# Kernel optimization log

Hardware: AMD Instinct MI355X
Metric: run time of the kernel (lower is better)

The kernel has to match this reference:

```python
import jax, jax.numpy as jnp
import numpy as np

B, T, C = 2, 2048, 1024
H, D, R = 16, 64, 32  # heads, head_dim, compression rank (R < D)


def setup_inputs() -> dict:
    key = jax.random.key(0)
    ks = jax.random.split(key, 8)
    s = 0.02
    return {
        "hidden_states": jax.random.normal(ks[0], (B, T, C), jnp.float32),
        "c_attn_w": jax.random.normal(ks[1], (C, 3 * C), jnp.float32) * s,
        "c_attn_b": jnp.zeros((3 * C,), jnp.float32),
        "c_proj_w": jax.random.normal(ks[2], (C, C), jnp.float32) * s,
        "c_proj_b": jnp.zeros((C,), jnp.float32),
        "wk_c": jax.random.normal(ks[3], (D, R), jnp.float32) * (1.0 / np.sqrt(D)),
        "wk_e": jax.random.normal(ks[4], (R, D), jnp.float32) * (1.0 / np.sqrt(R)),
        "wv_c": jax.random.normal(ks[5], (D, R), jnp.float32) * (1.0 / np.sqrt(D)),
        "wv_e": jax.random.normal(ks[6], (R, D), jnp.float32) * (1.0 / np.sqrt(R)),
    }


def reference(hidden_states, c_attn_w, c_attn_b, c_proj_w, c_proj_b,
              wk_c, wk_e, wv_c, wv_e):
    b, t, c = hidden_states.shape
    # GPT2 Conv1D: x @ W + b, then split into Q, K, V
    qkv = hidden_states @ c_attn_w + c_attn_b  # [B,T,3C]
    q, k, v = jnp.split(qkv, 3, axis=-1)

    def split_heads(x):  # [B,T,C] -> [B,H,T,D]
        return x.reshape(b, t, H, D).transpose(0, 2, 1, 3)

    q = split_heads(q)
    k = split_heads(k)
    v = split_heads(v)

    # Low-rank KV compression then expansion (rank R < D path)
    k_lat = jnp.einsum('bhtd,dr->bhtr', k, wk_c)  # [B,H,T,R]
    v_lat = jnp.einsum('bhtd,dr->bhtr', v, wv_c)
    k_exp = jnp.einsum('bhtr,rd->bhtd', k_lat, wk_e)  # [B,H,T,D]
    v_exp = jnp.einsum('bhtr,rd->bhtd', v_lat, wv_e)

    # Causal SDPA (attention_mask is None and q_len > 1 -> is_causal=True)
    scale = 1.0 / np.sqrt(D).astype(np.float32)
    scores = jnp.einsum('bhqd,bhkd->bhqk', q, k_exp) * scale  # [B,H,T,T]
    causal = jnp.tril(jnp.ones((t, t), dtype=bool))
    scores = jnp.where(causal[None, None], scores, jnp.finfo(scores.dtype).min)
    probs = jax.nn.softmax(scores, axis=-1)
    attn = jnp.einsum('bhqk,bhkd->bhqd', probs, v_exp)  # [B,H,T,D]

    # Merge heads and output projection
    attn = attn.transpose(0, 2, 1, 3).reshape(b, t, c)
    out = attn @ c_proj_w + c_proj_b
    return out
```

## Files before the change

### kernel.cpp

```cpp
#include <hip/hip_runtime.h>
#include <cstddef>

typedef __attribute__((ext_vector_type(8))) __bf16 bf16x8;
typedef __attribute__((ext_vector_type(4))) float f32x4;
typedef unsigned short u16;
typedef unsigned int   u32;

#define SCLF (0.125f * 1.44269504f)

__device__ __forceinline__ u16 f2bf(float f){
  union { float f; u32 u; } v; v.f = f;
  u32 r = v.u + 0x7FFFu + ((v.u >> 16) & 1u);
  return (u16)(r >> 16);
}
__device__ __forceinline__ u32 cvtpk(float lo, float hi){
  u32 r; asm("v_cvt_pk_bf16_f32 %0, %1, %2" : "=v"(r) : "v"(lo), "v"(hi)); return r;
}
__device__ __forceinline__ void gll16(const void* g, void* l){
  __builtin_amdgcn_global_load_lds((__attribute__((address_space(1))) void*)g,
                                   (__attribute__((address_space(3))) void*)l, 16, 0, 0);
}

__global__ void convert_x(const float* __restrict__ x, u16* __restrict__ o, int n4){
  int i = blockIdx.x*blockDim.x + threadIdx.x;
  if (i >= n4) return;
  float4 v = ((const float4*)x)[i];
  ushort4 r; r.x = f2bf(v.x); r.y = f2bf(v.y); r.z = f2bf(v.z); r.w = f2bf(v.w);
  ((ushort4*)o)[i] = r;
}

__global__ __launch_bounds__(256) void fold_qkvb(const float* __restrict__ Wa,
      const float* __restrict__ ba,
      const float* __restrict__ kc, const float* __restrict__ ke,
      const float* __restrict__ vc, u16* __restrict__ Wt, float* __restrict__ b2){
  __shared__ float WaL[64*65];
  __shared__ float Ws[2048];
  const int bid = blockIdx.x;
  const int tid = threadIdx.x;
  if (bid < 768){
    const int part = bid >> 8, rem = bid & 255, h = rem >> 4, cc = rem & 15;
    {
      const float* msrc = (part==0) ? ke : (part==1) ? kc : vc;
      *(float4*)&Ws[tid*4]        = ((const float4*)msrc)[tid];
      *(float4*)&Ws[1024 + tid*4] = ((const float4*)msrc)[tid + 256];
    }
    const int c0 = cc*64, off = part*1024 + h*64;
    {
      int r0 = tid >> 4, c4 = (tid & 15) * 4;
      #pragma unroll
      for (int i=0;i<4;++i){
        int row = i*16 + r0;
        float4 v = *(const float4*)&Wa[(size_t)(c0+row)*3072 + off + c4];
        WaL[row*65 + c4 + 0] = v.x;
        WaL[row*65 + c4 + 1] = v.y;
        WaL[row*65 + c4 + 2] = v.z;
        WaL[row*65 + c4 + 3] = v.w;
      }
    }
    __syncthreads();
    const int c = tid & 63, rg = tid >> 6;
    float acc[8] = {};
    if (part == 0){
      for (int d=0; d<64; ++d){
        float a = WaL[c*65 + d];
        #pragma unroll
        for (int rr=0;rr<8;++rr) acc[rr] += a * Ws[(rg*8+rr)*64 + d];
      }
    } else {
      for (int d=0; d<64; ++d){
        float a = WaL[c*65 + d];
        #pragma unroll
        for (int rr=0;rr<8;++rr) acc[rr] += a * Ws[d*32 + rg*8 + rr];
      }
    }
    const float scl = (part==0) ? SCLF : 1.f;
    const int nbase = part*512 + h*32 + rg*8;
    #pragma unroll
    for (int rr=0;rr<8;++rr)
      Wt[(size_t)(nbase+rr)*1024 + c0 + c] = f2bf(acc[rr]*scl);
  } else {
    const int part = bid - 768;
    float* BaL  = Ws;
    float* W65  = WaL;
    *(float4*)&BaL[tid*4] = *(const float4*)&ba[part*1024 + tid*4];
    {
      const float* msrc = (part==0) ? ke : (part==1) ? kc : vc;
      #pragma unroll
      for (int i=0;i<8;++i){
        int idx = tid + i*256;
        float v = msrc[idx];
        int r, d;
        if (part == 0){ r = idx >> 6; d = idx & 63; }
        else          { d = idx >> 5; r = idx & 31; }
        W65[r*65 + d] = v;
      }
    }
    __syncthreads();
    const float scl = (part==0) ? SCLF : 1.f;
    #pragma unroll
    for (int t=0;t<2;++t){
      int l = tid + t*256;
      int hh = l >> 5, r = l & 31;
      float acc = 0.f;
      for (int d=0;d<64;++d) acc += BaL[hh*64 + d] * W65[r*65 + d];
      b2[part*512 + l] = acc * scl;
    }
  }
}

__global__ __launch_bounds__(256) void fold_proj(const float* __restrict__ Wp,
      const float* __restrict__ ve, u16* __restrict__ W2t){
  __shared__ float WpL[8192];
  __shared__ float WeL[2048];
  const int jc = blockIdx.x, h = blockIdx.y;
  const int tid = threadIdx.x;
  {
    int dd = tid >> 5, c4 = (tid & 31) * 4;
    #pragma unroll
    for (int i=0;i<8;++i){
      int d = i*8 + dd;
      *(float4*)&WpL[d*128 + c4] = *(const float4*)&Wp[(size_t)(h*64+d)*1024 + jc*128 + c4];
    }
    *(float4*)&WeL[tid*4]        = ((const float4*)ve)[tid];
    *(float4*)&WeL[1024 + tid*4] = ((const float4*)ve)[tid + 256];
  }
  __syncthreads();
  const int jj = tid & 127, rg = tid >> 7;
  float out[16] = {};
  for (int d=0; d<64; ++d){
    float pv = WpL[d*128 + jj];
    #pragma unroll
    for (int rr=0; rr<16; ++rr) out[rr] += WeL[(rg*16+rr)*64 + d] * pv;
  }
  #pragma unroll
  for (int rr=0; rr<16; ++rr)
    W2t[(size_t)(jc*128 + jj)*512 + h*32 + rg*16 + rr] = f2bf(out[rr]);
}

template<typename OT>
__global__ __launch_bounds__(256) void gemm64(const u16* __restrict__ A, const u16* __restrict__ Bt,
        const float* __restrict__ bias, OT* __restrict__ C, u16* __restrict__ Vt,
        int M, int N, int K, int ldc){
  __shared__ u16 As[64*64];
  __shared__ u16 Bs[128*64];
  const int nwg = gridDim.x * gridDim.y;
  const int id  = blockIdx.x + gridDim.x * blockIdx.y;
  const int nid = (id & 7) * (nwg >> 3) + (id >> 3);
  const int bx = nid % gridDim.x, by = nid / gridDim.x;
  const int tid = threadIdx.x, wv = tid>>6, ln = tid&63;
  const int lr = ln&15, g8 = (ln>>4)*8;
  const int m0 = bx*64, n0 = by*128;
  const int wr = (wv>>1)*32, wc = (wv&1)*64;
  const int lrow = ln>>3, lcol = (ln&7)*8;
  f32x4 acc[2][4] = {};
  const int nk = K >> 6;
  for (int kt=0; kt<nk; ++kt){
    #pragma unroll
    for (int it=0; it<6; ++it){
      int chunk = wv*6 + it;
      if (chunk < 8){
        int row = chunk*8 + lrow;
        gll16(A + (size_t)(m0+row)*K + kt*64 + lcol, &As[chunk*512]);
      } else {
        int bc = chunk - 8;
        int row = bc*8 + lrow;
        gll16(Bt + (size_t)(n0+row)*K + kt*64 + lcol, &Bs[bc*512]);
      }
    }
    __syncthreads();
    #pragma unroll
    for (int ks=0; ks<2; ++ks){
      bf16x8 af[2], bfr[4];
      #pragma unroll
      for (int mt=0;mt<2;++mt) af[mt]  = *(const bf16x8*)&As[(wr+mt*16+lr)*64 + ks*32 + g8];
      #pragma unroll
      for (int nt=0;nt<4;++nt) bfr[nt] = *(const bf16x8*)&Bs[(wc+nt*16+lr)*64 + ks*32 + g8];
      #pragma unroll
      for (int mt=0;mt<2;++mt)
        #pragma unroll
        for (int nt=0;nt<4;++nt)
          acc[mt][nt] = __builtin_amdgcn_mfma_f32_16x16x32_bf16(af[mt], bfr[nt], acc[mt][nt], 0,0,0);
    }
    __syncthreads();
  }
  if (Vt && n0 >= 1024){
    #pragma unroll
    for (int mt=0;mt<2;++mt){
      int row0 = m0 + wr + mt*16 + 4*(ln>>4);
      int tin  = row0 & 2047;
      int p0 = 4*((tin>>4)&1) + 8*((tin>>2)&3) + 32*(tin>>5);
      size_t vbase = (size_t)(row0 >> 11) * 512;
      #pragma unroll
      for (int nt=0;nt<4;++nt){
        int col = n0 + wc + nt*16 + lr;
        float bv = bias[col];
        int nlat = col - 1024;
        union { u16 s[4]; uint2 v; } pk;
        #pragma unroll
        for (int r=0;r<4;++r) pk.s[r] = f2bf(acc[mt][nt][r] + bv);
        *(uint2*)&Vt[(vbase + nlat)*2048 + p0] = pk.v;
      }
    }
  } else {
    #pragma unroll
    for (int mt=0;mt<2;++mt){
      int row = m0 + wr + mt*16 + 4*(ln>>4);
      #pragma unroll
      for (int nt=0;nt<4;++nt){
        int col = n0 + wc + nt*16 + lr;
        float bv = bias[col];
        #pragma unroll
        for (int r=0;r<4;++r){
          float v = acc[mt][nt][r] + bv;
          if constexpr (sizeof(OT) == 2) C[(size_t)(row+r)*ldc + col] = f2bf(v);
          else                           C[(size_t)(row+r)*ldc + col] = v;
        }
      }
    }
  }
}

__global__ __launch_bounds__(512, 8) void attn_fwd(const u16* __restrict__ QKV,
            const u16* __restrict__ Vt, u16* __restrict__ Out){
  const int bh = blockIdx.x;
  const int qt = 31 - blockIdx.y;
  const int b = bh >> 4, h = bh & 15;
  const int tid = threadIdx.x, wv = tid>>6, ln = tid&63;
  const int sg = wv>>2, wvL = wv&3;
  const int lr = ln&15, gq = ln>>4;
  __shared__ __align__(16) char SMEM[32768];
  u16* KB0 = (u16*)SMEM           + (sg*2    )*2048;
  u16* KB1 = (u16*)SMEM           + (sg*2 + 1)*2048;
  u16* VB0 = (u16*)(SMEM + 16384) + (sg*2    )*2048;
  u16* VB1 = (u16*)(SMEM + 16384) + (sg*2 + 1)*2048;
  const int q0 = qt*64;
  const size_t base = (size_t)(b*2048) * 1536;
  bf16x8 qf = *(const bf16x8*)(QKV + base + (size_t)(q0 + wvL*16 + lr)*1536 + h*32 + gq*8);
  const int qglob = q0 + wvL*16 + lr;
  f32x4 o0 = {}, o1 = {};
  float l_r = 0.f;
  const u16* ksrc = QKV + base + 512 + h*32;
  const u16* vsrc = Vt + (size_t)(bh*32)*2048;

  const int ci = wvL*64 + ln;
  const int rK = ci>>2, cK = 8*((ci&3) ^ (rK&3));
  const int rV = ci>>3, cV = 8*((ci&7) ^ (rV&7));

  int offK[4], offV[2][2];
  #pragma unroll
  for (int nt=0;nt<4;++nt)
    offK[nt] = (nt*16+lr)*64 + ((gq*16) ^ ((lr&3)<<4));
  #pragma unroll
  for (int dt=0;dt<2;++dt)
    #pragma unroll
    for (int c=0;c<2;++c)
      offV[dt][c] = (dt*16+lr)*128 + ((c*64 + gq*16) ^ ((lr&7)<<4));

  if (sg <= qt){
    gll16(ksrc + (size_t)(sg*64 + rK)*1536 + cK, KB0 + wvL*512);
    gll16(vsrc + (size_t)rV*2048 + sg*64 + cV,   VB0 + wvL*512);
  }
  __syncthreads();
  const u16* kp = ksrc + (size_t)(sg*64 + 128 + rK)*1536 + cK;
  const u16* vp = vsrc + (size_t)rV*2048 + sg*64 + 128 + cV;
  const size_t KSTEP = (size_t)128*1536;

  #define ABODY(II, KBC, VBC, KBN, VBN) do { \
    const int kt = 2*(II) + sg; \
    if (kt + 2 <= qt){ \
      gll16(kp, (KBN) + wvL*512); \
      gll16(vp, (VBN) + wvL*512); \
      kp += KSTEP; vp += 128; \
    } \
    if (kt <= qt){ \
      f32x4 s4[4] = {}; \
      __builtin_amdgcn_s_setprio(1); \
      _Pragma("unroll") for (int nt=0;nt<4;++nt){ \
        bf16x8 k0 = *(const bf16x8*)((const char*)(KBC) + offK[nt]); \
        s4[nt] = __builtin_amdgcn_mfma_f32_16x16x32_bf16(k0, qf, s4[nt], 0,0,0); \
      } \
      __builtin_amdgcn_s_setprio(0); \
      if (kt == qt){ \
        const int kv0 = kt*64; \
        _Pragma("unroll") for (int nt=0;nt<4;++nt) \
        _Pragma("unroll") for (int r=0;r<4;++r){ \
          int k = kv0 + nt*16 + 4*gq + r; \
          if (k > qglob) s4[nt][r] = -1e30f; \
        } \
      } \
      float p0,p1,p2,p3,p4,p5,p6,p7; \
      p0=__builtin_amdgcn_exp2f(s4[0][0]); p1=__builtin_amdgcn_exp2f(s4[0][1]); \
      p2=__builtin_amdgcn_exp2f(s4[0][2]); p3=__builtin_amdgcn_exp2f(s4[0][3]); \
      p4=__builtin_amdgcn_exp2f(s4[1][0]); p5=__builtin_amdgcn_exp2f(s4[1][1]); \
      p6=__builtin_amdgcn_exp2f(s4[1][2]); p7=__builtin_amdgcn_exp2f(s4[1][3]); \
      l_r += ((p0+p1)+(p2+p3)) + ((p4+p5)+(p6+p7)); \
      union { u32 u[4]; bf16x8 v; } pa0, pa1; \
      pa0.u[0]=cvtpk(p0,p1); pa0.u[1]=cvtpk(p2,p3); pa0.u[2]=cvtpk(p4,p5); pa0.u[3]=cvtpk(p6,p7); \
      p0=__builtin_amdgcn_exp2f(s4[2][0]); p1=__builtin_amdgcn_exp2f(s4[2][1]); \
      p2=__builtin_amdgcn_exp2f(s4[2][2]); p3=__builtin_amdgcn_exp2f(s4[2][3]); \
      p4=__builtin_amdgcn_exp2f(s4[3][0]); p5=__builtin_amdgcn_exp2f(s4[3][1]); \
      p6=__builtin_amdgcn_exp2f(s4[3][2]); p7=__builtin_amdgcn_exp2f(s4[3][3]); \
      l_r += ((p0+p1)+(p2+p3)) + ((p4+p5)+(p6+p7)); \
      pa1.u[0]=cvtpk(p0,p1); pa1.u[1]=cvtpk(p2,p3); pa1.u[2]=cvtpk(p4,p5); pa1.u[3]=cvtpk(p6,p7); \
      __builtin_amdgcn_s_setprio(1); \
      o0 = __builtin_amdgcn_mfma_f32_16x16x32_bf16(pa0.v, *(const bf16x8*)((const char*)(VBC) + offV[0][0]), o0, 0,0,0); \
      o1 = __builtin_amdgcn_mfma_f32_16x16x32_bf16(pa0.v, *(const bf16x8*)((const char*)(VBC) + offV[1][0]), o1, 0,0,0); \
      o0 = __builtin_amdgcn_mfma_f32_16x16x32_bf16(pa1.v, *(const bf16x8*)((const char*)(VBC) + offV[0][1]), o0, 0,0,0); \
      o1 = __builtin_amdgcn_mfma_f32_16x16x32_bf16(pa1.v, *(const bf16x8*)((const char*)(VBC) + offV[1][1]), o1, 0,0,0); \
      __builtin_amdgcn_s_setprio(0); \
    } \
    __syncthreads(); \
  } while(0)

  const int nmax = (qt + 2) >> 1;
  const int jmax = (nmax + 1) >> 1;
  for (int j = 0; j < jmax; ++j){
    ABODY(2*j,   KB0, VB0, KB1, VB1);
    ABODY(2*j+1, KB1, VB1, KB0, VB0);
  }
  l_r += __shfl_xor(l_r, 16);
  l_r += __shfl_xor(l_r, 32);

  float* MO = (float*)SMEM;
  float* ML = (float*)(SMEM + 12288);
  if (sg == 1){
    #pragma unroll
    for (int r=0;r<4;++r){
      MO[(wvL*16 + 4*gq + r)*34 + lr]      = o0[r];
      MO[(wvL*16 + 4*gq + r)*34 + 16 + lr] = o1[r];
    }
    if (gq == 0) ML[wvL*16 + lr] = l_r;
  }
  __syncthreads();
  if (sg == 0){
    float lS = l_r + ML[wvL*16 + lr];
    float lS_o[4];
    #pragma unroll
    for (int r=0;r<4;++r) lS_o[r] = __shfl(lS, 4*gq + r);
    #pragma unroll
    for (int r=0;r<4;++r){
      int orow = wvL*16 + 4*gq + r;
      float v0 = (o0[r] + MO[orow*34 + lr])      / lS_o[r];
      float v1 = (o1[r] + MO[orow*34 + 16 + lr]) / lS_o[r];
      size_t ob = (size_t)(b*2048 + q0 + orow)*512 + h*32;
      Out[ob + lr]      = f2bf(v0);
      Out[ob + 16 + lr] = f2bf(v1);
    }
  }
}

#define WS_B2   0u
#define WS_WT   8192u
#define WS_W2T  (WS_WT + 3145728u)
#define WS_XB   (WS_W2T + 1048576u)
#define WS_QKV  (WS_XB + 8388608u)
#define WS_VT   (WS_QKV + 12582912u)
#define WS_ATT  (WS_VT + 4194304u)

extern "C" void kernel_launch(void* const* d_in, const int* in_sizes, int n_in,
                              void* d_out, int out_size, void* d_ws, size_t ws_size,
                              hipStream_t stream) {
  const float* x  = (const float*)d_in[0];
  const float* Wa = (const float*)d_in[1];
  const float* ba = (const float*)d_in[2];
  const float* Wp = (const float*)d_in[3];
  const float* bp = (const float*)d_in[4];
  const float* kc = (const float*)d_in[5];
  const float* ke = (const float*)d_in[6];
  const float* vc = (const float*)d_in[7];
  const float* ve = (const float*)d_in[8];
  float* out = (float*)d_out;
  char* ws = (char*)d_ws;
  float* b2  = (float*)(ws + WS_B2);
  u16* Wt    = (u16*)(ws + WS_WT);
  u16* W2t   = (u16*)(ws + WS_W2T);
  u16* Xb    = (u16*)(ws + WS_XB);
  u16* QKVb  = (u16*)(ws + WS_QKV);
  u16* Vt    = (u16*)(ws + WS_VT);
  u16* Att   = (u16*)(ws + WS_ATT);

  convert_x<<<4096, 256, 0, stream>>>(x, Xb, 1048576);
  fold_qkvb<<<771, 256, 0, stream>>>(Wa, ba, kc, ke, vc, Wt, b2);
  fold_proj<<<dim3(8,16), 256, 0, stream>>>(Wp, ve, W2t);
  gemm64<u16><<<dim3(64,12), 256, 0, stream>>>(Xb, Wt, b2, QKVb, Vt, 4096, 1536, 1024, 1536);
  attn_fwd<<<dim3(32,32), 512, 0, stream>>>(QKVb, Vt, Att);
  gemm64<float><<<dim3(64,8), 256, 0, stream>>>(Att, W2t, bp, out, (u16*)nullptr, 4096, 1024, 512, 1024);
}
```

Baseline: 85.64 us.

## Move weight folding to bf16 MFMA GEMMs and merge conversion kernels

```diff
diff --git a/kernel.cpp b/kernel.cpp
--- a/kernel.cpp
+++ b/kernel.cpp
@@ -21,67 +21,37 @@
                                    (__attribute__((address_space(3))) void*)l, 16, 0, 0);
 }
 
-__global__ void convert_x(const float* __restrict__ x, u16* __restrict__ o, int n4){
-  int i = blockIdx.x*blockDim.x + threadIdx.x;
-  if (i >= n4) return;
-  float4 v = ((const float4*)x)[i];
-  ushort4 r; r.x = f2bf(v.x); r.y = f2bf(v.y); r.z = f2bf(v.z); r.w = f2bf(v.w);
-  ((ushort4*)o)[i] = r;
-}
-
-__global__ __launch_bounds__(256) void fold_qkvb(const float* __restrict__ Wa,
-      const float* __restrict__ ba,
+__global__ __launch_bounds__(256) void convert_all(const float* __restrict__ x,
+      const float* __restrict__ Wa, const float* __restrict__ ba,
       const float* __restrict__ kc, const float* __restrict__ ke,
-      const float* __restrict__ vc, u16* __restrict__ Wt, float* __restrict__ b2){
-  __shared__ float WaL[64*65];
-  __shared__ float Ws[2048];
-  const int bid = blockIdx.x;
-  const int tid = threadIdx.x;
-  if (bid < 768){
-    const int part = bid >> 8, rem = bid & 255, h = rem >> 4, cc = rem & 15;
-    {
-      const float* msrc = (part==0) ? ke : (part==1) ? kc : vc;
-      *(float4*)&Ws[tid*4]        = ((const float4*)msrc)[tid];
-      *(float4*)&Ws[1024 + tid*4] = ((const float4*)msrc)[tid + 256];
-    }
-    const int c0 = cc*64, off = part*1024 + h*64;
-    {
-      int r0 = tid >> 4, c4 = (tid & 15) * 4;
-      #pragma unroll
-      for (int i=0;i<4;++i){
-        int row = i*16 + r0;
-        float4 v = *(const float4*)&Wa[(size_t)(c0+row)*3072 + off + c4];
-        WaL[row*65 + c4 + 0] = v.x;
-        WaL[row*65 + c4 + 1] = v.y;
-        WaL[row*65 + c4 + 2] = v.z;
-        WaL[row*65 + c4 + 3] = v.w;
-      }
-    }
-    __syncthreads();
-    const int c = tid & 63, rg = tid >> 6;
-    float acc[8] = {};
-    if (part == 0){
-      for (int d=0; d<64; ++d){
-        float a = WaL[c*65 + d];
-        #pragma unroll
-        for (int rr=0;rr<8;++rr) acc[rr] += a * Ws[(rg*8+rr)*64 + d];
-      }
-    } else {
-      for (int d=0; d<64; ++d){
-        float a = WaL[c*65 + d];
-        #pragma unroll
-        for (int rr=0;rr<8;++rr) acc[rr] += a * Ws[d*32 + rg*8 + rr];
-      }
-    }
-    const float scl = (part==0) ? SCLF : 1.f;
-    const int nbase = part*512 + h*32 + rg*8;
-    #pragma unroll
-    for (int rr=0;rr<8;++rr)
-      Wt[(size_t)(nbase+rr)*1024 + c0 + c] = f2bf(acc[rr]*scl);
+      const float* __restrict__ vc, const float* __restrict__ ve,
+      u16* __restrict__ Xb, u16* __restrict__ Wab, u16* __restrict__ Mb,
+      float* __restrict__ b2){
+  __shared__ float BaL[1024];
+  __shared__ float W65[32*65];
+  const int bid = blockIdx.x, tid = threadIdx.x;
+  if (bid < 4096){
+    int i = bid*256 + tid;
+    float4 v = ((const float4*)x)[i];
+    ushort4 r; r.x=f2bf(v.x); r.y=f2bf(v.y); r.z=f2bf(v.z); r.w=f2bf(v.w);
+    ((ushort4*)Xb)[i] = r;
+  } else if (bid < 7168){
+    int i = (bid-4096)*256 + tid;
+    float4 v = ((const float4*)Wa)[i];
+    ushort4 r; r.x=f2bf(v.x); r.y=f2bf(v.y); r.z=f2bf(v.z); r.w=f2bf(v.w);
+    ((ushort4*)Wab)[i] = r;
+  } else if (bid == 7168){
+    #pragma unroll
+    for (int t=0;t<8;++t){
+      int idx = t*256 + tid;
+      Mb[idx] = f2bf(ke[idx]*SCLF);
+      int d = idx>>5, r = idx&31;
+      Mb[2048 + r*64 + d] = f2bf(kc[idx]);
+      Mb[4096 + r*64 + d] = f2bf(vc[idx]);
+      Mb[6144 + idx] = f2bf(ve[idx]);
+    }
   } else {
-    const int part = bid - 768;
-    float* BaL  = Ws;
-    float* W65  = WaL;
+    const int part = bid - 7169;
     *(float4*)&BaL[tid*4] = *(const float4*)&ba[part*1024 + tid*4];
     {
       const float* msrc = (part==0) ? ke : (part==1) ? kc : vc;
@@ -108,33 +78,97 @@
   }
 }
 
-__global__ __launch_bounds__(256) void fold_proj(const float* __restrict__ Wp,
-      const float* __restrict__ ve, u16* __restrict__ W2t){
-  __shared__ float WpL[8192];
-  __shared__ float WeL[2048];
-  const int jc = blockIdx.x, h = blockIdx.y;
-  const int tid = threadIdx.x;
-  {
-    int dd = tid >> 5, c4 = (tid & 31) * 4;
-    #pragma unroll
-    for (int i=0;i<8;++i){
-      int d = i*8 + dd;
-      *(float4*)&WpL[d*128 + c4] = *(const float4*)&Wp[(size_t)(h*64+d)*1024 + jc*128 + c4];
-    }
-    *(float4*)&WeL[tid*4]        = ((const float4*)ve)[tid];
-    *(float4*)&WeL[1024 + tid*4] = ((const float4*)ve)[tid + 256];
+__global__ __launch_bounds__(256) void transpose_cvt(const float* __restrict__ src, int ld_src,
+            u16* __restrict__ dst, int ld_dst){
+  __shared__ float tile[64][65];
+  int c0 = blockIdx.x*64, n0 = blockIdx.y*64;
+  int tx = threadIdx.x & 63, ty = threadIdx.x >> 6;
+  #pragma unroll 4
+  for (int k=0;k<16;++k){
+    int r = 4*k + ty;
+    tile[r][tx] = src[(size_t)(c0+r)*ld_src + n0 + tx];
   }
   __syncthreads();
-  const int jj = tid & 127, rg = tid >> 7;
-  float out[16] = {};
-  for (int d=0; d<64; ++d){
-    float pv = WpL[d*128 + jj];
-    #pragma unroll
-    for (int rr=0; rr<16; ++rr) out[rr] += WeL[(rg*16+rr)*64 + d] * pv;
-  }
-  #pragma unroll
-  for (int rr=0; rr<16; ++rr)
-    W2t[(size_t)(jc*128 + jj)*512 + h*32 + rg*16 + rr] = f2bf(out[rr]);
+  #pragma unroll 4
+  for (int k=0;k<16;++k){
+    int r = 4*k + ty;
+    dst[(size_t)(n0+r)*ld_dst + c0 + tx] = f2bf(tile[tx][r]);
+  }
+}
+
+__global__ __launch_bounds__(256) void fold_gemm_qkv(const u16* __restrict__ Wab,
+      const u16* __restrict__ Mb, u16* __restrict__ Wt){
+  __shared__ u16 As[4096];
+  __shared__ u16 Bs[2048];
+  const int cc = blockIdx.x, ph = blockIdx.y;
+  const int tid = threadIdx.x, wv = tid>>6, ln = tid&63;
+  const int lr = ln&15, g8 = (ln>>4)*8, gq = ln>>4;
+  const int c0 = cc*64;
+  const u16* A = Wab + (size_t)c0*3072 + ph*64;
+  const u16* B = Mb + (ph>>4)*2048;
+  const int lrow = ln>>3, lcol = (ln&7)*8;
+  #pragma unroll
+  for (int it=0;it<3;++it){
+    int c3 = wv*3 + it;
+    if (c3 < 8) gll16(A + (size_t)(c3*8+lrow)*3072 + lcol, &As[c3*512]);
+    else { int bc = c3-8; gll16(B + (bc*8+lrow)*64 + lcol, &Bs[bc*512]); }
+  }
+  __syncthreads();
+  f32x4 acc[2] = {};
+  const int wr = (wv>>1)*32, wn = wv&1;
+  #pragma unroll
+  for (int ks=0;ks<2;++ks){
+    bf16x8 bf = *(const bf16x8*)&Bs[(wn*16+lr)*64 + ks*32 + g8];
+    #pragma unroll
+    for (int mt=0;mt<2;++mt){
+      bf16x8 af = *(const bf16x8*)&As[(wr+mt*16+lr)*64 + ks*32 + g8];
+      acc[mt] = __builtin_amdgcn_mfma_f32_16x16x32_bf16(af, bf, acc[mt], 0,0,0);
+    }
+  }
+  const int n = (ph>>4)*512 + (ph&15)*32 + wn*16 + lr;
+  #pragma unroll
+  for (int mt=0;mt<2;++mt){
+    union { u16 s[4]; uint2 v; } pk;
+    #pragma unroll
+    for (int r=0;r<4;++r) pk.s[r] = f2bf(acc[mt][r]);
+    *(uint2*)&Wt[(size_t)n*1024 + c0 + wr + mt*16 + 4*gq] = pk.v;
+  }
+}
+
+__global__ __launch_bounds__(256) void fold_gemm_proj(const u16* __restrict__ WpTb,
+      const u16* __restrict__ veb, u16* __restrict__ W2t){
+  __shared__ u16 As[4096];
+  __shared__ u16 Bs[2048];
+  const int cc = blockIdx.x, ph = blockIdx.y;
+  const int tid = threadIdx.x, wv = tid>>6, ln = tid&63;
+  const int lr = ln&15, g8 = (ln>>4)*8, gq = ln>>4;
+  const int c0 = cc*64;
+  const u16* A = WpTb + (size_t)c0*1024 + ph*64;
+  const int lrow = ln>>3, lcol = (ln&7)*8;
+  #pragma unroll
+  for (int it=0;it<3;++it){
+    int c3 = wv*3 + it;
+    if (c3 < 8) gll16(A + (size_t)(c3*8+lrow)*1024 + lcol, &As[c3*512]);
+    else { int bc = c3-8; gll16(veb + (bc*8+lrow)*64 + lcol, &Bs[bc*512]); }
+  }
+  __syncthreads();
+  f32x4 acc[2] = {};
+  const int wr = (wv>>1)*32, wn = wv&1;
+  #pragma unroll
+  for (int ks=0;ks<2;++ks){
+    bf16x8 bf = *(const bf16x8*)&Bs[(wn*16+lr)*64 + ks*32 + g8];
+    #pragma unroll
+    for (int mt=0;mt<2;++mt){
+      bf16x8 af = *(const bf16x8*)&As[(wr+mt*16+lr)*64 + ks*32 + g8];
+      acc[mt] = __builtin_amdgcn_mfma_f32_16x16x32_bf16(af, bf, acc[mt], 0,0,0);
+    }
+  }
+  const int col = ph*32 + wn*16 + lr;
+  #pragma unroll
+  for (int mt=0;mt<2;++mt)
+    #pragma unroll
+    for (int r=0;r<4;++r)
+      W2t[(size_t)(c0 + wr + mt*16 + 4*gq + r)*512 + col] = f2bf(acc[mt][r]);
 }
 
 template<typename OT>
@@ -356,6 +390,9 @@
 #define WS_QKV  (WS_XB + 8388608u)
 #define WS_VT   (WS_QKV + 12582912u)
 #define WS_ATT  (WS_VT + 4194304u)
+#define WS_WAB  (WS_ATT + 4194304u)
+#define WS_WPT  (WS_WAB + 6291456u)
+#define WS_MB   (WS_WPT + 2097152u)
 
 extern "C" void kernel_launch(void* const* d_in, const int* in_sizes, int n_in,
                               void* d_out, int out_size, void* d_ws, size_t ws_size,
@@ -378,10 +415,15 @@
   u16* QKVb  = (u16*)(ws + WS_QKV);
   u16* Vt    = (u16*)(ws + WS_VT);
   u16* Att   = (u16*)(ws + WS_ATT);
-
-  convert_x<<<4096, 256, 0, stream>>>(x, Xb, 1048576);
-  fold_qkvb<<<771, 256, 0, stream>>>(Wa, ba, kc, ke, vc, Wt, b2);
-  fold_proj<<<dim3(8,16), 256, 0, stream>>>(Wp, ve, W2t);
+  u16* Wab   = (u16*)(ws + WS_WAB);
+  u16* WpTb  = (u16*)(ws + WS_WPT);
+  u16* Mb    = (u16*)(ws + WS_MB);
+  u16* veb   = Mb + 6144;
+
+  convert_all<<<7172, 256, 0, stream>>>(x, Wa, ba, kc, ke, vc, ve, Xb, Wab, Mb, b2);
+  transpose_cvt<<<dim3(16,16), 256, 0, stream>>>(Wp, 1024, WpTb, 1024);
+  fold_gemm_qkv<<<dim3(16,48), 256, 0, stream>>>(Wab, Mb, Wt);
+  fold_gemm_proj<<<dim3(16,16), 256, 0, stream>>>(WpTb, veb, W2t);
   gemm64<u16><<<dim3(64,12), 256, 0, stream>>>(Xb, Wt, b2, QKVb, Vt, 4096, 1536, 1024, 1536);
   attn_fwd<<<dim3(32,32), 512, 0, stream>>>(QKVb, Vt, Att);
   gemm64<float><<<dim3(64,8), 256, 0, stream>>>(Att, W2t, bp, out, (u16*)nullptr, 4096, 1024, 512, 1024);
```

Result: no change. 84.13 us (-1.8%).
